# Optimization experiments

Hardware: AMD Instinct MI355X
Metric: run time of the kernel (lower is better)

## Reference

```python
import jax, jax.numpy as jnp
import numpy as np

CONF_W, POS_W, LEN_W, TRIG_W, CONST_W = 1.0, 1.0, 0.1, 1.0, 0.5
FOCAL_THR = 0.1
EPS = 6e-08


def setup_inputs() -> dict:
    key = jax.random.key(0)
    k1, k2, k3, k4, k5 = jax.random.split(key, 5)
    B, C, H, W = 32, 10, 192, 320
    u = jax.random.uniform(k1, (B, H, W), dtype=jnp.float32)
    gt0 = jnp.where(u > 0.95, 1.0, u * 2.0 - 1.0)
    gt_rest = jax.random.normal(k2, (B, C - 1, H, W), dtype=jnp.float32) * 0.5
    gt = jnp.concatenate([gt0[:, None], gt_rest], axis=1)
    # re channel 0: confidence strictly in (0,1) so logs are finite
    re0 = jax.random.uniform(k3, (B, 1, H, W), dtype=jnp.float32, minval=0.05, maxval=0.95)
    re_rest = jax.random.normal(k4, (B, C - 1, H, W), dtype=jnp.float32) * 0.5
    re = jnp.concatenate([re0, re_rest], axis=1)
    return {"re": re, "gt": gt}


def _smooth_l1(d):
    ad = jnp.abs(d)
    return jnp.where(ad < 1.0, 0.5 * d * d, ad - 0.5)


def _forward(re, gt):
    gt0 = gt[:, 0]  # [B,H,W]
    re0 = re[:, 0]
    m0 = gt0 >= 0.0            # confidence mask (above 0)
    mv = gt0 == 1.0            # vehicle mask
    m0f = m0.astype(jnp.float32)
    mvf = mv.astype(jnp.float32)
    nv = mvf.sum()             # number of vehicle pixels (one channel)

    def mse2(rc, gc):
        # mean over two masked channels
        s = sum(((re[:, r] - gt[:, g]) ** 2 * mvf).sum() for r, g in zip(rc, gc))
        return s / (2.0 * nv)

    def sl1_2(rc, gc):
        s = sum((_smooth_l1(re[:, r] - gt[:, g]) * mvf).sum() for r, g in zip(rc, gc))
        return s / (2.0 * nv)

    # focal confidence loss (threshold 0.1) over pixels with gt0 >= 0
    pos = m0f * (gt0 >= FOCAL_THR).astype(jnp.float32)
    neg = m0f * (gt0 < FOCAL_THR).astype(jnp.float32)
    num_pos = pos.sum()
    safe_re = jnp.clip(re0, 1e-6, 1.0 - 1e-6)  # masked-out entries must not NaN
    pos_term = -(pos * (gt0 - re0) ** 2 * jnp.log(safe_re + EPS)).sum()
    neg_term = -(neg * re0 ** 2 * jnp.log(1.0 + EPS - safe_re) * (1.0 - gt0) ** 4).sum()
    focal = jnp.where(num_pos == 0.0, neg_term, (pos_term + neg_term) / num_pos)

    confidence_loss = CONF_W * focal
    pos_loss = POS_W * sl1_2([1, 2], [1, 2])
    length_v1 = LEN_W * sl1_2([3, 6], [3, 6])
    length_v2 = LEN_W * sl1_2([3, 6], [6, 3])
    trig_v1 = TRIG_W * (mse2([4, 7], [4, 7]) + mse2([5, 8], [5, 8]))
    trig_v2 = TRIG_W * (mse2([4, 7], [7, 4]) + mse2([5, 8], [8, 5]))

    const1 = (((1.0 - re[:, 5] ** 2 - re[:, 4] ** 2) ** 2) * mvf).sum() / nv
    const2 = (((1.0 - re[:, 8] ** 2 - re[:, 7] ** 2) ** 2) * mvf).sum() / nv
    const_loss = CONST_W * (const1 + const2)

    height_loss = LEN_W * (_smooth_l1(re[:, 9] - gt[:, 9]) * mvf).sum() / nv

    dimensions_loss = jnp.minimum(length_v1 + trig_v1, length_v2 + trig_v2) + height_loss
    return confidence_loss + pos_loss + dimensions_loss + const_loss


def reference(re, gt):
    return _forward(re, gt)
```

## Files before the change

### kernel.cpp

```cpp
#include <hip/hip_runtime.h>
#include <math.h>

constexpr int B_ = 32, C_ = 10, H_ = 192, W_ = 320;
constexpr int HW_  = H_ * W_;
constexpr int CHW_ = C_ * HW_;
constexpr int NPTS = B_ * HW_;
constexpr int NV4  = NPTS / 4;
constexpr int NBLK = NV4 / 256;

#define NACC 7

__device__ __forceinline__ float sl1f(float d) {
    float ad = fabsf(d);
    return ad < 1.0f ? 0.5f * d * d : ad - 0.5f;
}

__global__ __launch_bounds__(256, 2) void loss_main(
    const float* __restrict__ re, const float* __restrict__ gt,
    float* __restrict__ ws)
{
    const int tid = blockIdx.x * 256 + threadIdx.x;
    const int p = tid * 4;
    const int b = p / HW_;
    const int s = p - b * HW_;
    const float* rp = re + (size_t)b * CHW_ + s;
    const float* gp = gt + (size_t)b * CHW_ + s;

    float4 R[10], G[10];
#pragma unroll
    for (int c = 0; c < 10; ++c) {
        R[c] = *(const float4*)(rp + c * HW_);
        G[c] = *(const float4*)(gp + c * HW_);
    }
    __builtin_amdgcn_sched_barrier(0);

    float acc[NACC];
#pragma unroll
    for (int i = 0; i < NACC; ++i) acc[i] = 0.0f;

#pragma unroll
    for (int j = 0; j < 4; ++j) {
        #define RC(c) (((const float*)&R[c])[j])
        #define GC(c) (((const float*)&G[c])[j])
        const float g = GC(0), r = RC(0);
        const float m = (g == 1.0f) ? 1.0f : 0.0f;
        acc[0] += m;
        const float pos = (g >= 0.1f) ? 1.0f : 0.0f;
        const float neg = ((g >= 0.0f) && (g < 0.1f)) ? 1.0f : 0.0f;
        acc[1] += pos;
        const float safe = fminf(fmaxf(r, 1e-6f), 1.0f - 1e-6f);
        const float d0 = g - r;
        acc[2] += pos * (d0 * d0) * logf(safe + 6e-8f);
        const float omg = 1.0f - g;
        const float omg2 = omg * omg;
        acc[3] += neg * (r * r) * logf(1.0f + 6e-8f - safe) * (omg2 * omg2);

        const float r1 = RC(1), r2 = RC(2), r3 = RC(3), r4v = RC(4);
        const float r5 = RC(5), r6 = RC(6), r7 = RC(7), r8 = RC(8), r9 = RC(9);
        const float g1 = GC(1), g2 = GC(2), g3 = GC(3), g4v = GC(4);
        const float g5 = GC(5), g6 = GC(6), g7 = GC(7), g8 = GC(8), g9 = GC(9);

        const float sp = sl1f(r1 - g1) + sl1f(r2 - g2);
        const float c1 = 1.0f - r5 * r5 - r4v * r4v;
        const float c2 = 1.0f - r8 * r8 - r7 * r7;
        const float sc = c1 * c1 + c2 * c2;
        const float sh = sl1f(r9 - g9);
        acc[4] += m * (0.5f * sp + 0.5f * sc + 0.1f * sh);

        const float d44 = r4v - g4v, d77 = r7 - g7;
        const float d55 = r5 - g5,  d88 = r8 - g8;
        const float t1 = d44 * d44 + d77 * d77 + d55 * d55 + d88 * d88;
        const float l1 = sl1f(r3 - g3) + sl1f(r6 - g6);
        acc[5] += m * (0.05f * l1 + 0.5f * t1);

        const float d47 = r4v - g7, d74 = r7 - g4v;
        const float d58 = r5 - g8,  d85 = r8 - g5;
        const float t2 = d47 * d47 + d74 * d74 + d58 * d58 + d85 * d85;
        const float l2 = sl1f(r3 - g6) + sl1f(r6 - g3);
        acc[6] += m * (0.05f * l2 + 0.5f * t2);
        #undef RC
        #undef GC
    }

    __shared__ float smem[NACC][4];
    const int lane = threadIdx.x & 63;
    const int wid  = threadIdx.x >> 6;
#pragma unroll
    for (int i = 0; i < NACC; ++i) {
        float v = acc[i];
#pragma unroll
        for (int off = 32; off > 0; off >>= 1) v += __shfl_down(v, off, 64);
        if (lane == 0) smem[i][wid] = v;
    }
    __syncthreads();
    if (threadIdx.x < NACC) {
        const int i = threadIdx.x;
        ws[i * NBLK + blockIdx.x] =
            smem[i][0] + smem[i][1] + smem[i][2] + smem[i][3];
    }
}

__global__ __launch_bounds__(1024) void loss_reduce(
    const float* __restrict__ ws, float* __restrict__ out)
{
    float acc[NACC];
#pragma unroll
    for (int i = 0; i < NACC; ++i) acc[i] = 0.0f;

#pragma unroll
    for (int k = 0; k < 2; ++k) {
        const int idx = threadIdx.x + k * 1024;
        if (idx < NBLK) {
#pragma unroll
            for (int i = 0; i < NACC; ++i)
                acc[i] += ws[i * NBLK + idx];
        }
    }

    __shared__ float smem[NACC][16];
    const int lane = threadIdx.x & 63;
    const int wid  = threadIdx.x >> 6;
#pragma unroll
    for (int i = 0; i < NACC; ++i) {
        float v = acc[i];
#pragma unroll
        for (int off = 32; off > 0; off >>= 1) v += __shfl_down(v, off, 64);
        if (lane == 0) smem[i][wid] = v;
    }
    __syncthreads();

    if (threadIdx.x == 0) {
        float slot[NACC];
#pragma unroll
        for (int i = 0; i < NACC; ++i) {
            float v = 0.0f;
#pragma unroll
            for (int w = 0; w < 16; ++w) v += smem[i][w];
            slot[i] = v;
        }
        const float nv    = slot[0];
        const float npos  = slot[1];
        const float pterm = -slot[2];
        const float nterm = -slot[3];
        const float focal = (npos == 0.0f) ? nterm : (pterm + nterm) / npos;
        out[0] = focal + (slot[4] + fminf(slot[5], slot[6])) / nv;
    }
}

extern "C" void kernel_launch(void* const* d_in, const int* in_sizes, int n_in,
                              void* d_out, int out_size, void* d_ws, size_t ws_size,
                              hipStream_t stream)
{
    const float* re = (const float*)d_in[0];
    const float* gt = (const float*)d_in[1];
    float* ws  = (float*)d_ws;
    float* out = (float*)d_out;

    loss_main<<<NBLK, 256, 0, stream>>>(re, gt, ws);
    loss_reduce<<<1, 1024, 0, stream>>>(ws, out);
}
```

Baseline: 176.0 us.

## Split loss work into channel-group blocks so each block loads fewer channels

The single fused kernel, where each thread loaded all 20 channel float4s, becomes five channel-group block types, each loading only its channels plus gt channel 0. Each block covers a 512-float4 slice of one image over two iterations, and the reduce kernel now reads the larger block count. The aim is to cut register pressure and raise occupancy and memory-level parallelism. In exchange, gt channel 0 is re-read by every group, blocks take divergent paths, and more partial sums must be reduced.

```diff
diff --git a/kernel.cpp b/kernel.cpp
--- a/kernel.cpp
+++ b/kernel.cpp
@@ -3,10 +3,14 @@
 
 constexpr int B_ = 32, C_ = 10, H_ = 192, W_ = 320;
 constexpr int HW_  = H_ * W_;
+constexpr int HW4_ = HW_ / 4;
 constexpr int CHW_ = C_ * HW_;
-constexpr int NPTS = B_ * HW_;
-constexpr int NV4  = NPTS / 4;
-constexpr int NBLK = NV4 / 256;
+constexpr int SLICE4 = 512;
+constexpr int T_  = SLICE4 / 256;
+constexpr int SPI = HW4_ / SLICE4;
+constexpr int BPG = B_ * SPI;
+constexpr int NGRP = 5;
+constexpr int NBLK = NGRP * BPG;
 
 #define NACC 7
 
@@ -15,71 +19,118 @@
     return ad < 1.0f ? 0.5f * d * d : ad - 0.5f;
 }
 
-__global__ __launch_bounds__(256, 2) void loss_main(
+__global__ __launch_bounds__(256) void loss_main(
     const float* __restrict__ re, const float* __restrict__ gt,
     float* __restrict__ ws)
 {
-    const int tid = blockIdx.x * 256 + threadIdx.x;
-    const int p = tid * 4;
-    const int b = p / HW_;
-    const int s = p - b * HW_;
-    const float* rp = re + (size_t)b * CHW_ + s;
-    const float* gp = gt + (size_t)b * CHW_ + s;
-
-    float4 R[10], G[10];
-#pragma unroll
-    for (int c = 0; c < 10; ++c) {
-        R[c] = *(const float4*)(rp + c * HW_);
-        G[c] = *(const float4*)(gp + c * HW_);
-    }
-    __builtin_amdgcn_sched_barrier(0);
+    const int grp = blockIdx.x % NGRP;
+    const int wb  = blockIdx.x / NGRP;
+    const int img = wb / SPI;
+    const int sl  = wb - img * SPI;
+    const float* rbase = re + (size_t)img * CHW_;
+    const float* gbase = gt + (size_t)img * CHW_;
+    const int f0 = sl * SLICE4 * 4;
 
     float acc[NACC];
 #pragma unroll
     for (int i = 0; i < NACC; ++i) acc[i] = 0.0f;
 
-#pragma unroll
-    for (int j = 0; j < 4; ++j) {
-        #define RC(c) (((const float*)&R[c])[j])
-        #define GC(c) (((const float*)&G[c])[j])
-        const float g = GC(0), r = RC(0);
-        const float m = (g == 1.0f) ? 1.0f : 0.0f;
-        acc[0] += m;
-        const float pos = (g >= 0.1f) ? 1.0f : 0.0f;
-        const float neg = ((g >= 0.0f) && (g < 0.1f)) ? 1.0f : 0.0f;
-        acc[1] += pos;
-        const float safe = fminf(fmaxf(r, 1e-6f), 1.0f - 1e-6f);
-        const float d0 = g - r;
-        acc[2] += pos * (d0 * d0) * logf(safe + 6e-8f);
-        const float omg = 1.0f - g;
-        const float omg2 = omg * omg;
-        acc[3] += neg * (r * r) * logf(1.0f + 6e-8f - safe) * (omg2 * omg2);
-
-        const float r1 = RC(1), r2 = RC(2), r3 = RC(3), r4v = RC(4);
-        const float r5 = RC(5), r6 = RC(6), r7 = RC(7), r8 = RC(8), r9 = RC(9);
-        const float g1 = GC(1), g2 = GC(2), g3 = GC(3), g4v = GC(4);
-        const float g5 = GC(5), g6 = GC(6), g7 = GC(7), g8 = GC(8), g9 = GC(9);
-
-        const float sp = sl1f(r1 - g1) + sl1f(r2 - g2);
-        const float c1 = 1.0f - r5 * r5 - r4v * r4v;
-        const float c2 = 1.0f - r8 * r8 - r7 * r7;
-        const float sc = c1 * c1 + c2 * c2;
-        const float sh = sl1f(r9 - g9);
-        acc[4] += m * (0.5f * sp + 0.5f * sc + 0.1f * sh);
-
-        const float d44 = r4v - g4v, d77 = r7 - g7;
-        const float d55 = r5 - g5,  d88 = r8 - g8;
-        const float t1 = d44 * d44 + d77 * d77 + d55 * d55 + d88 * d88;
-        const float l1 = sl1f(r3 - g3) + sl1f(r6 - g6);
-        acc[5] += m * (0.05f * l1 + 0.5f * t1);
-
-        const float d47 = r4v - g7, d74 = r7 - g4v;
-        const float d58 = r5 - g8,  d85 = r8 - g5;
-        const float t2 = d47 * d47 + d74 * d74 + d58 * d58 + d85 * d85;
-        const float l2 = sl1f(r3 - g6) + sl1f(r6 - g3);
-        acc[6] += m * (0.05f * l2 + 0.5f * t2);
-        #undef RC
-        #undef GC
+    if (grp == 0) {
+        for (int t = 0; t < T_; ++t) {
+            const int s = f0 + (t * 256 + threadIdx.x) * 4;
+            const float4 G0 = *(const float4*)(gbase + s);
+            const float4 R0 = *(const float4*)(rbase + s);
+#pragma unroll
+            for (int j = 0; j < 4; ++j) {
+                const float g = ((const float*)&G0)[j];
+                const float r = ((const float*)&R0)[j];
+                acc[0] += (g == 1.0f) ? 1.0f : 0.0f;
+                const float pos = (g >= 0.1f) ? 1.0f : 0.0f;
+                const float neg = ((g >= 0.0f) && (g < 0.1f)) ? 1.0f : 0.0f;
+                acc[1] += pos;
+                const float safe = fminf(fmaxf(r, 1e-6f), 1.0f - 1e-6f);
+                const float d0 = g - r;
+                acc[2] += pos * (d0 * d0) * logf(safe + 6e-8f);
+                const float omg = 1.0f - g;
+                const float omg2 = omg * omg;
+                acc[3] += neg * (r * r) * logf(1.0f + 6e-8f - safe) * (omg2 * omg2);
+            }
+        }
+    } else if (grp == 1) {
+        for (int t = 0; t < T_; ++t) {
+            const int s = f0 + (t * 256 + threadIdx.x) * 4;
+            const float4 G0 = *(const float4*)(gbase + s);
+            const float4 R1 = *(const float4*)(rbase + s + 1 * HW_);
+            const float4 G1 = *(const float4*)(gbase + s + 1 * HW_);
+            const float4 R2 = *(const float4*)(rbase + s + 2 * HW_);
+            const float4 G2 = *(const float4*)(gbase + s + 2 * HW_);
+#pragma unroll
+            for (int j = 0; j < 4; ++j) {
+                const float m = (((const float*)&G0)[j] == 1.0f) ? 1.0f : 0.0f;
+                const float sp = sl1f(((const float*)&R1)[j] - ((const float*)&G1)[j])
+                               + sl1f(((const float*)&R2)[j] - ((const float*)&G2)[j]);
+                acc[4] += m * 0.5f * sp;
+            }
+        }
+    } else if (grp == 2) {
+        for (int t = 0; t < T_; ++t) {
+            const int s = f0 + (t * 256 + threadIdx.x) * 4;
+            const float4 G0 = *(const float4*)(gbase + s);
+            const float4 R3 = *(const float4*)(rbase + s + 3 * HW_);
+            const float4 G3 = *(const float4*)(gbase + s + 3 * HW_);
+            const float4 R6 = *(const float4*)(rbase + s + 6 * HW_);
+            const float4 G6 = *(const float4*)(gbase + s + 6 * HW_);
+#pragma unroll
+            for (int j = 0; j < 4; ++j) {
+                const float m = (((const float*)&G0)[j] == 1.0f) ? 1.0f : 0.0f;
+                const float r3 = ((const float*)&R3)[j], g3 = ((const float*)&G3)[j];
+                const float r6 = ((const float*)&R6)[j], g6 = ((const float*)&G6)[j];
+                acc[5] += m * 0.05f * (sl1f(r3 - g3) + sl1f(r6 - g6));
+                acc[6] += m * 0.05f * (sl1f(r3 - g6) + sl1f(r6 - g3));
+            }
+        }
+    } else if (grp == 3) {
+        for (int t = 0; t < T_; ++t) {
+            const int s = f0 + (t * 256 + threadIdx.x) * 4;
+            const float4 G0 = *(const float4*)(gbase + s);
+            const float4 R4 = *(const float4*)(rbase + s + 4 * HW_);
+            const float4 G4 = *(const float4*)(gbase + s + 4 * HW_);
+            const float4 R5 = *(const float4*)(rbase + s + 5 * HW_);
+            const float4 G5 = *(const float4*)(gbase + s + 5 * HW_);
+            const float4 R7 = *(const float4*)(rbase + s + 7 * HW_);
+            const float4 G7 = *(const float4*)(gbase + s + 7 * HW_);
+            const float4 R8 = *(const float4*)(rbase + s + 8 * HW_);
+            const float4 G8 = *(const float4*)(gbase + s + 8 * HW_);
+#pragma unroll
+            for (int j = 0; j < 4; ++j) {
+                const float m = (((const float*)&G0)[j] == 1.0f) ? 1.0f : 0.0f;
+                const float r4 = ((const float*)&R4)[j], g4 = ((const float*)&G4)[j];
+                const float r5 = ((const float*)&R5)[j], g5 = ((const float*)&G5)[j];
+                const float r7 = ((const float*)&R7)[j], g7 = ((const float*)&G7)[j];
+                const float r8 = ((const float*)&R8)[j], g8 = ((const float*)&G8)[j];
+                const float d44 = r4 - g4, d77 = r7 - g7;
+                const float d55 = r5 - g5, d88 = r8 - g8;
+                acc[5] += m * 0.5f * (d44 * d44 + d77 * d77 + d55 * d55 + d88 * d88);
+                const float d47 = r4 - g7, d74 = r7 - g4;
+                const float d58 = r5 - g8, d85 = r8 - g5;
+                acc[6] += m * 0.5f * (d47 * d47 + d74 * d74 + d58 * d58 + d85 * d85);
+                const float c1 = 1.0f - r5 * r5 - r4 * r4;
+                const float c2 = 1.0f - r8 * r8 - r7 * r7;
+                acc[4] += m * 0.5f * (c1 * c1 + c2 * c2);
+            }
+        }
+    } else {
+        for (int t = 0; t < T_; ++t) {
+            const int s = f0 + (t * 256 + threadIdx.x) * 4;
+            const float4 G0 = *(const float4*)(gbase + s);
+            const float4 R9 = *(const float4*)(rbase + s + 9 * HW_);
+            const float4 G9 = *(const float4*)(gbase + s + 9 * HW_);
+#pragma unroll
+            for (int j = 0; j < 4; ++j) {
+                const float m = (((const float*)&G0)[j] == 1.0f) ? 1.0f : 0.0f;
+                acc[4] += m * 0.1f * sl1f(((const float*)&R9)[j] - ((const float*)&G9)[j]);
+            }
+        }
     }
 
     __shared__ float smem[NACC][4];
@@ -108,7 +159,7 @@
     for (int i = 0; i < NACC; ++i) acc[i] = 0.0f;
 
 #pragma unroll
-    for (int k = 0; k < 2; ++k) {
+    for (int k = 0; k < 5; ++k) {
         const int idx = threadIdx.x + k * 1024;
         if (idx < NBLK) {
 #pragma unroll
```

New measurement: 178.8 us. No clear change (+1.6%).

## Split loss work per channel across threads, each looping over several batches

Applied to the files above, without the earlier changes.

Instead of one thread loading all ten channels of re and gt for four pixels, each thread now handles one channel slot and loops over eight batch images, with branches per channel group. Work is spread over many more threads and register pressure drops, which is meant to improve occupancy and memory-level parallelism. In exchange, the mask channel and some partner channels are loaded redundantly by many threads, which raises total memory traffic. Branches are uniform within a wavefront only where channel boundaries align, and the reduce kernel now reads a third chunk of partial sums.

```diff
diff --git a/kernel.cpp b/kernel.cpp
--- a/kernel.cpp
+++ b/kernel.cpp
@@ -1,12 +1,16 @@
 #include <hip/hip_runtime.h>
 #include <math.h>
 
-constexpr int B_ = 32, C_ = 10, H_ = 192, W_ = 320;
-constexpr int HW_  = H_ * W_;
-constexpr int CHW_ = C_ * HW_;
-constexpr int NPTS = B_ * HW_;
-constexpr int NV4  = NPTS / 4;
-constexpr int NBLK = NV4 / 256;
+constexpr int B_    = 32, C_ = 10, H_ = 192, W_ = 320;
+constexpr int HW_   = H_ * W_;
+constexpr int HW4_  = HW_ / 4;
+constexpr int CHW_  = C_ * HW_;
+constexpr int CHW4_ = CHW_ / 4;
+constexpr int N4_   = B_ * CHW4_;
+constexpr int T_    = 8;
+constexpr int NTHR  = N4_ / T_;
+constexpr int NBLK  = NTHR / 256;
+constexpr int BSTEP = NTHR / CHW4_;
 
 #define NACC 7
 
@@ -15,72 +19,122 @@
     return ad < 1.0f ? 0.5f * d * d : ad - 0.5f;
 }
 
-__global__ __launch_bounds__(256, 2) void loss_main(
+__global__ __launch_bounds__(256) void loss_main(
     const float* __restrict__ re, const float* __restrict__ gt,
     float* __restrict__ ws)
 {
-    const int tid = blockIdx.x * 256 + threadIdx.x;
-    const int p = tid * 4;
-    const int b = p / HW_;
-    const int s = p - b * HW_;
-    const float* rp = re + (size_t)b * CHW_ + s;
-    const float* gp = gt + (size_t)b * CHW_ + s;
-
-    float4 R[10], G[10];
-#pragma unroll
-    for (int c = 0; c < 10; ++c) {
-        R[c] = *(const float4*)(rp + c * HW_);
-        G[c] = *(const float4*)(gp + c * HW_);
-    }
-    __builtin_amdgcn_sched_barrier(0);
+    const int tid  = blockIdx.x * 256 + threadIdx.x;
+    const int b0   = tid / CHW4_;
+    const int slot = tid - b0 * CHW4_;
+    const int c    = slot / HW4_;
+    const int hw   = (slot - c * HW4_) * 4;
+
+    const size_t base = (size_t)b0 * CHW_ + (size_t)c * HW_ + hw;
+    const float* gch = gt + base;
+    const float* rch = re + base;
+    const float* g0p = gt + (size_t)b0 * CHW_ + hw;
+    constexpr size_t STEP = (size_t)BSTEP * CHW_;
 
     float acc[NACC];
 #pragma unroll
     for (int i = 0; i < NACC; ++i) acc[i] = 0.0f;
 
-#pragma unroll
-    for (int j = 0; j < 4; ++j) {
-        #define RC(c) (((const float*)&R[c])[j])
-        #define GC(c) (((const float*)&G[c])[j])
-        const float g = GC(0), r = RC(0);
-        const float m = (g == 1.0f) ? 1.0f : 0.0f;
-        acc[0] += m;
-        const float pos = (g >= 0.1f) ? 1.0f : 0.0f;
-        const float neg = ((g >= 0.0f) && (g < 0.1f)) ? 1.0f : 0.0f;
-        acc[1] += pos;
-        const float safe = fminf(fmaxf(r, 1e-6f), 1.0f - 1e-6f);
-        const float d0 = g - r;
-        acc[2] += pos * (d0 * d0) * logf(safe + 6e-8f);
-        const float omg = 1.0f - g;
-        const float omg2 = omg * omg;
-        acc[3] += neg * (r * r) * logf(1.0f + 6e-8f - safe) * (omg2 * omg2);
-
-        const float r1 = RC(1), r2 = RC(2), r3 = RC(3), r4v = RC(4);
-        const float r5 = RC(5), r6 = RC(6), r7 = RC(7), r8 = RC(8), r9 = RC(9);
-        const float g1 = GC(1), g2 = GC(2), g3 = GC(3), g4v = GC(4);
-        const float g5 = GC(5), g6 = GC(6), g7 = GC(7), g8 = GC(8), g9 = GC(9);
-
-        const float sp = sl1f(r1 - g1) + sl1f(r2 - g2);
-        const float c1 = 1.0f - r5 * r5 - r4v * r4v;
-        const float c2 = 1.0f - r8 * r8 - r7 * r7;
-        const float sc = c1 * c1 + c2 * c2;
-        const float sh = sl1f(r9 - g9);
-        acc[4] += m * (0.5f * sp + 0.5f * sc + 0.1f * sh);
-
-        const float d44 = r4v - g4v, d77 = r7 - g7;
-        const float d55 = r5 - g5,  d88 = r8 - g8;
-        const float t1 = d44 * d44 + d77 * d77 + d55 * d55 + d88 * d88;
-        const float l1 = sl1f(r3 - g3) + sl1f(r6 - g6);
-        acc[5] += m * (0.05f * l1 + 0.5f * t1);
-
-        const float d47 = r4v - g7, d74 = r7 - g4v;
-        const float d58 = r5 - g8,  d85 = r8 - g5;
-        const float t2 = d47 * d47 + d74 * d74 + d58 * d58 + d85 * d85;
-        const float l2 = sl1f(r3 - g6) + sl1f(r6 - g3);
-        acc[6] += m * (0.05f * l2 + 0.5f * t2);
-        #undef RC
-        #undef GC
-    }
+    #define ELEM(v) (((const float*)&v)[j])
+
+    if (c == 0) {
+        for (int k = 0; k < T_; ++k) {
+            const float4 G = *(const float4*)(gch + k * STEP);
+            const float4 R = *(const float4*)(rch + k * STEP);
+#pragma unroll
+            for (int j = 0; j < 4; ++j) {
+                const float g = ELEM(G), r = ELEM(R);
+                acc[0] += (g == 1.0f) ? 1.0f : 0.0f;
+                const float pos = (g >= 0.1f) ? 1.0f : 0.0f;
+                const float neg = ((g >= 0.0f) && (g < 0.1f)) ? 1.0f : 0.0f;
+                acc[1] += pos;
+                const float safe = fminf(fmaxf(r, 1e-6f), 1.0f - 1e-6f);
+                const float d0 = g - r;
+                acc[2] += pos * (d0 * d0) * logf(safe + 6e-8f);
+                const float omg = 1.0f - g;
+                const float omg2 = omg * omg;
+                acc[3] += neg * (r * r) * logf(1.0f + 6e-8f - safe) * (omg2 * omg2);
+            }
+        }
+    } else if (c == 1 || c == 2) {
+        for (int k = 0; k < T_; ++k) {
+            const float4 M = *(const float4*)(g0p + k * STEP);
+            const float4 G = *(const float4*)(gch + k * STEP);
+            const float4 R = *(const float4*)(rch + k * STEP);
+#pragma unroll
+            for (int j = 0; j < 4; ++j) {
+                const float m = (ELEM(M) == 1.0f) ? 1.0f : 0.0f;
+                acc[4] += m * 0.5f * sl1f(ELEM(R) - ELEM(G));
+            }
+        }
+    } else if (c == 3 || c == 6) {
+        const float* gxp = (c == 3) ? gch + 3 * HW_ : gch - 3 * HW_;
+        for (int k = 0; k < T_; ++k) {
+            const float4 M  = *(const float4*)(g0p + k * STEP);
+            const float4 G  = *(const float4*)(gch + k * STEP);
+            const float4 R  = *(const float4*)(rch + k * STEP);
+            const float4 GX = *(const float4*)(gxp + k * STEP);
+#pragma unroll
+            for (int j = 0; j < 4; ++j) {
+                const float m = (ELEM(M) == 1.0f) ? 1.0f : 0.0f;
+                acc[5] += m * 0.05f * sl1f(ELEM(R) - ELEM(G));
+                acc[6] += m * 0.05f * sl1f(ELEM(R) - ELEM(GX));
+            }
+        }
+    } else if (c == 4 || c == 7) {
+        const float* gxp = (c == 4) ? gch + 3 * HW_ : gch - 3 * HW_;
+        for (int k = 0; k < T_; ++k) {
+            const float4 M  = *(const float4*)(g0p + k * STEP);
+            const float4 G  = *(const float4*)(gch + k * STEP);
+            const float4 R  = *(const float4*)(rch + k * STEP);
+            const float4 GX = *(const float4*)(gxp + k * STEP);
+#pragma unroll
+            for (int j = 0; j < 4; ++j) {
+                const float m = (ELEM(M) == 1.0f) ? 1.0f : 0.0f;
+                const float d1 = ELEM(R) - ELEM(G);
+                const float d2 = ELEM(R) - ELEM(GX);
+                acc[5] += m * 0.5f * d1 * d1;
+                acc[6] += m * 0.5f * d2 * d2;
+            }
+        }
+    } else if (c == 5 || c == 8) {
+        const float* gxp = (c == 5) ? gch + 3 * HW_ : gch - 3 * HW_;
+        const float* rxp = rch - HW_;
+        for (int k = 0; k < T_; ++k) {
+            const float4 M  = *(const float4*)(g0p + k * STEP);
+            const float4 G  = *(const float4*)(gch + k * STEP);
+            const float4 R  = *(const float4*)(rch + k * STEP);
+            const float4 GX = *(const float4*)(gxp + k * STEP);
+            const float4 RX = *(const float4*)(rxp + k * STEP);
+#pragma unroll
+            for (int j = 0; j < 4; ++j) {
+                const float m = (ELEM(M) == 1.0f) ? 1.0f : 0.0f;
+                const float r = ELEM(R), rx = ELEM(RX);
+                const float d1 = r - ELEM(G);
+                const float d2 = r - ELEM(GX);
+                acc[5] += m * 0.5f * d1 * d1;
+                acc[6] += m * 0.5f * d2 * d2;
+                const float cc = 1.0f - r * r - rx * rx;
+                acc[4] += m * 0.5f * cc * cc;
+            }
+        }
+    } else {
+        for (int k = 0; k < T_; ++k) {
+            const float4 M = *(const float4*)(g0p + k * STEP);
+            const float4 G = *(const float4*)(gch + k * STEP);
+            const float4 R = *(const float4*)(rch + k * STEP);
+#pragma unroll
+            for (int j = 0; j < 4; ++j) {
+                const float m = (ELEM(M) == 1.0f) ? 1.0f : 0.0f;
+                acc[4] += m * 0.1f * sl1f(ELEM(R) - ELEM(G));
+            }
+        }
+    }
+    #undef ELEM
 
     __shared__ float smem[NACC][4];
     const int lane = threadIdx.x & 63;
@@ -108,7 +162,7 @@
     for (int i = 0; i < NACC; ++i) acc[i] = 0.0f;
 
 #pragma unroll
-    for (int k = 0; k < 2; ++k) {
+    for (int k = 0; k < 3; ++k) {
         const int idx = threadIdx.x + k * 1024;
         if (idx < NBLK) {
 #pragma unroll
```

Measured after the change: 178.4 us. No clear change (+1.3%).

## Fuse final reduction into main kernel via last-block atomic counter

Applied to the files above, without the earlier changes.

Replaces the separate single-block reduce kernel with a last-block-done pattern: each block writes its partials, bumps an atomic counter after a fence, and the final block sums all partials and writes the result. A memset of the counter is added before the launch. It also drops the occupancy hint of two blocks per SM and the scheduling barrier after the loads. This removes one kernel launch but adds a memset, atomics, fences, and a serial tail reduction in a single 256-thread block.

```diff
diff --git a/kernel.cpp b/kernel.cpp
--- a/kernel.cpp
+++ b/kernel.cpp
@@ -1,7 +1,7 @@
 #include <hip/hip_runtime.h>
 #include <math.h>
 
-constexpr int B_ = 32, C_ = 10, H_ = 192, W_ = 320;
+constexpr int B_   = 32, C_ = 10, H_ = 192, W_ = 320;
 constexpr int HW_  = H_ * W_;
 constexpr int CHW_ = C_ * HW_;
 constexpr int NPTS = B_ * HW_;
@@ -15,9 +15,10 @@
     return ad < 1.0f ? 0.5f * d * d : ad - 0.5f;
 }
 
-__global__ __launch_bounds__(256, 2) void loss_main(
+__global__ __launch_bounds__(256) void loss_fused(
     const float* __restrict__ re, const float* __restrict__ gt,
-    float* __restrict__ ws)
+    float* __restrict__ ws, int* __restrict__ counter,
+    float* __restrict__ out)
 {
     const int tid = blockIdx.x * 256 + threadIdx.x;
     const int p = tid * 4;
@@ -32,7 +33,6 @@
         R[c] = *(const float4*)(rp + c * HW_);
         G[c] = *(const float4*)(gp + c * HW_);
     }
-    __builtin_amdgcn_sched_barrier(0);
 
     float acc[NACC];
 #pragma unroll
@@ -83,14 +83,12 @@
     }
 
     __shared__ float smem[NACC][4];
-    const int lane = threadIdx.x & 63;
-    const int wid  = threadIdx.x >> 6;
 #pragma unroll
     for (int i = 0; i < NACC; ++i) {
         float v = acc[i];
 #pragma unroll
         for (int off = 32; off > 0; off >>= 1) v += __shfl_down(v, off, 64);
-        if (lane == 0) smem[i][wid] = v;
+        if ((threadIdx.x & 63) == 0) smem[i][threadIdx.x >> 6] = v;
     }
     __syncthreads();
     if (threadIdx.x < NACC) {
@@ -98,46 +96,43 @@
         ws[i * NBLK + blockIdx.x] =
             smem[i][0] + smem[i][1] + smem[i][2] + smem[i][3];
     }
-}
+    __syncthreads();
 
-__global__ __launch_bounds__(1024) void loss_reduce(
-    const float* __restrict__ ws, float* __restrict__ out)
-{
-    float acc[NACC];
+    __shared__ int is_last;
+    if (threadIdx.x == 0) {
+        __threadfence();
+        const int old = atomicAdd(counter, 1);
+        is_last = (old == NBLK - 1) ? 1 : 0;
+    }
+    __syncthreads();
+    if (!is_last) return;
+
+    __threadfence();
+
+    float racc[NACC];
 #pragma unroll
-    for (int i = 0; i < NACC; ++i) acc[i] = 0.0f;
-
+    for (int i = 0; i < NACC; ++i) racc[i] = 0.0f;
+    for (int idx = threadIdx.x; idx < NBLK; idx += 256) {
 #pragma unroll
-    for (int k = 0; k < 2; ++k) {
-        const int idx = threadIdx.x + k * 1024;
-        if (idx < NBLK) {
-#pragma unroll
-            for (int i = 0; i < NACC; ++i)
-                acc[i] += ws[i * NBLK + idx];
-        }
+        for (int i = 0; i < NACC; ++i)
+            racc[i] += ws[i * NBLK + idx];
     }
 
-    __shared__ float smem[NACC][16];
-    const int lane = threadIdx.x & 63;
-    const int wid  = threadIdx.x >> 6;
+    __syncthreads();
 #pragma unroll
     for (int i = 0; i < NACC; ++i) {
-        float v = acc[i];
+        float v = racc[i];
 #pragma unroll
         for (int off = 32; off > 0; off >>= 1) v += __shfl_down(v, off, 64);
-        if (lane == 0) smem[i][wid] = v;
+        if ((threadIdx.x & 63) == 0) smem[i][threadIdx.x >> 6] = v;
     }
     __syncthreads();
 
     if (threadIdx.x == 0) {
         float slot[NACC];
 #pragma unroll
-        for (int i = 0; i < NACC; ++i) {
-            float v = 0.0f;
-#pragma unroll
-            for (int w = 0; w < 16; ++w) v += smem[i][w];
-            slot[i] = v;
-        }
+        for (int i = 0; i < NACC; ++i)
+            slot[i] = smem[i][0] + smem[i][1] + smem[i][2] + smem[i][3];
         const float nv    = slot[0];
         const float npos  = slot[1];
         const float pterm = -slot[2];
@@ -153,9 +148,10 @@
 {
     const float* re = (const float*)d_in[0];
     const float* gt = (const float*)d_in[1];
-    float* ws  = (float*)d_ws;
-    float* out = (float*)d_out;
+    float* ws   = (float*)d_ws;
+    int* counter = (int*)((float*)d_ws + NACC * NBLK);
+    float* out  = (float*)d_out;
 
-    loss_main<<<NBLK, 256, 0, stream>>>(re, gt, ws);
-    loss_reduce<<<1, 1024, 0, stream>>>(ws, out);
+    hipMemsetAsync(counter, 0, sizeof(int), stream);
+    loss_fused<<<NBLK, 256, 0, stream>>>(re, gt, ws, counter, out);
 }
```

Result: slower. 274.8 us (+56.1%).
